# Optimization experiments

Measured on AMD Instinct MI355X. Metric: run time of the kernel, lower is better.

## Reference

```python
import jax, jax.numpy as jnp
import numpy as np

USER_NUM = 200000
ITEM_NUM = 100000
EMB = 64
N_LAYERS = 2
NE_S = 3200000
NE_R = 3200000


def setup_inputs() -> dict:
    key = jax.random.key(0)
    ks = jax.random.split(key, 10)
    scale = 1.0 / np.sqrt(EMB)
    user_emb = jax.random.normal(ks[0], (USER_NUM, EMB), jnp.float32) * scale
    item_emb = jax.random.normal(ks[1], (ITEM_NUM, EMB), jnp.float32) * scale
    # torch Linear weight is [out_features, in_features] = [EMB, 2*EMB]
    W = jax.random.normal(ks[2], (N_LAYERS, EMB, 2 * EMB), jnp.float32) * (1.0 / np.sqrt(2 * EMB))
    b = jnp.zeros((N_LAYERS, EMB), jnp.float32)
    s_rows = jax.random.randint(ks[3], (NE_S,), 0, USER_NUM, jnp.int32)
    s_cols = jax.random.randint(ks[4], (NE_S,), 0, USER_NUM, jnp.int32)
    s_vals = jax.random.uniform(ks[5], (NE_S,), jnp.float32) / 16.0  # ~row-normalized
    r_rows = jax.random.randint(ks[6], (NE_R,), 0, USER_NUM, jnp.int32)
    r_cols = jax.random.randint(ks[7], (NE_R,), 0, ITEM_NUM, jnp.int32)
    r_vals = jax.random.uniform(ks[8], (NE_R,), jnp.float32) / 16.0
    return {"user_emb": user_emb, "item_emb": item_emb, "W": W, "b": b,
            "s_rows": s_rows, "s_cols": s_cols, "s_vals": s_vals,
            "r_rows": r_rows, "r_cols": r_cols, "r_vals": r_vals}


def _spmm(rows, cols, vals, X, n_rows):
    # COO sparse [n_rows, n_cols] @ dense X[n_cols, d]
    return jax.ops.segment_sum(vals[:, None] * X[cols], rows, num_segments=n_rows)


def reference(user_emb, item_emb, W, b, s_rows, s_cols, s_vals, r_rows, r_cols, r_vals):
    U = user_emb
    V = item_emb
    for i in range(N_LAYERS):
        agg = _spmm(s_rows, s_cols, s_vals, U, USER_NUM)      # [U, EMB]
        h = jnp.concatenate([agg, U], axis=1)                 # [U, 2*EMB]
        U = jax.nn.relu(h @ W[i].T + b[i])                    # [U, EMB]
    user_all = U + _spmm(r_rows, r_cols, r_vals, V, USER_NUM)
    item_all = V
    return (user_all, item_all)
```

## Files before the change

kernel.cpp:

```cpp
#include <hip/hip_runtime.h>

#define USER_NUM 200000
#define ITEM_NUM 100000
#define EMB 64

#define SCAN_T 256
#define SCAN_E 8
#define SCAN_TILE (SCAN_T * SCAN_E)

__global__ __launch_bounds__(256) void hist_kernel(
    const int* __restrict__ rows, int nnz, int* __restrict__ cnt)
{
    int e = blockIdx.x * 256 + threadIdx.x;
    if (e >= nnz) return;
    atomicAdd(&cnt[rows[e]], 1);
}

__global__ __launch_bounds__(SCAN_T) void block_sum_kernel(
    const int* __restrict__ cnt, int n, int* __restrict__ partials)
{
    __shared__ int sm[SCAN_T];
    int tid = threadIdx.x;
    int base = blockIdx.x * SCAN_TILE + tid * SCAN_E;
    int s = 0;
    #pragma unroll
    for (int j = 0; j < SCAN_E; ++j) {
        int i = base + j;
        if (i < n) s += cnt[i];
    }
    sm[tid] = s; __syncthreads();
    for (int off = SCAN_T / 2; off > 0; off >>= 1) {
        if (tid < off) sm[tid] += sm[tid + off];
        __syncthreads();
    }
    if (tid == 0) partials[blockIdx.x] = sm[0];
}

__global__ __launch_bounds__(SCAN_T) void scan_partials_kernel(
    int* __restrict__ partials, int nblocks)
{
    __shared__ int sm[SCAN_T];
    int tid = threadIdx.x;
    int v = (tid < nblocks) ? partials[tid] : 0;
    sm[tid] = v; __syncthreads();
    for (int off = 1; off < SCAN_T; off <<= 1) {
        int a = (tid >= off) ? sm[tid - off] : 0;
        __syncthreads();
        sm[tid] += a;
        __syncthreads();
    }
    if (tid < nblocks) partials[tid] = sm[tid] - v;
}

__global__ __launch_bounds__(SCAN_T) void scan_tile_kernel(
    const int* __restrict__ cnt, int n, const int* __restrict__ partials,
    int* __restrict__ row_ptr, int* __restrict__ cursor)
{
    __shared__ int sm[SCAN_T];
    int tid = threadIdx.x;
    int base = blockIdx.x * SCAN_TILE + tid * SCAN_E;
    int local[SCAN_E];
    int s = 0;
    #pragma unroll
    for (int j = 0; j < SCAN_E; ++j) {
        int i = base + j;
        local[j] = (i < n) ? cnt[i] : 0;
        s += local[j];
    }
    sm[tid] = s; __syncthreads();
    for (int off = 1; off < SCAN_T; off <<= 1) {
        int a = (tid >= off) ? sm[tid - off] : 0;
        __syncthreads();
        sm[tid] += a;
        __syncthreads();
    }
    int run = partials[blockIdx.x] + (sm[tid] - s);
    #pragma unroll
    for (int j = 0; j < SCAN_E; ++j) {
        int i = base + j;
        if (i < n) { row_ptr[i] = run; cursor[i] = run; }
        run += local[j];
        if (i == n - 1) row_ptr[n] = run;
    }
}

__global__ __launch_bounds__(256) void scatter_kernel(
    const int* __restrict__ rows, const int* __restrict__ cols,
    const float* __restrict__ vals, int nnz,
    int* __restrict__ cursor, int2* __restrict__ epairs)
{
    int e = blockIdx.x * 256 + threadIdx.x;
    if (e >= nnz) return;
    int r = rows[e];
    int p = atomicAdd(&cursor[r], 1);
    epairs[p] = make_int2(cols[e], __float_as_int(vals[e]));
}

__global__ __launch_bounds__(256) void spmm_csr_kernel(
    const int* __restrict__ row_ptr, const int2* __restrict__ epairs,
    const float* __restrict__ X, const float* __restrict__ addin,
    float* __restrict__ out, int n_rows)
{
    int gid = blockIdx.x * 256 + threadIdx.x;
    int row = gid >> 6;
    int lane = gid & 63;
    if (row >= n_rows) return;
    int beg = row_ptr[row], end = row_ptr[row + 1];
    float acc = addin ? addin[(size_t)row * EMB + lane] : 0.0f;
    int i = beg;
    for (; i + 4 <= end; i += 4) {
        int2 e0 = epairs[i], e1 = epairs[i+1], e2 = epairs[i+2], e3 = epairs[i+3];
        float x0 = X[(size_t)e0.x * EMB + lane];
        float x1 = X[(size_t)e1.x * EMB + lane];
        float x2 = X[(size_t)e2.x * EMB + lane];
        float x3 = X[(size_t)e3.x * EMB + lane];
        acc = fmaf(__int_as_float(e0.y), x0, acc);
        acc = fmaf(__int_as_float(e1.y), x1, acc);
        acc = fmaf(__int_as_float(e2.y), x2, acc);
        acc = fmaf(__int_as_float(e3.y), x3, acc);
    }
    for (; i < end; ++i) {
        int2 e = epairs[i];
        acc = fmaf(__int_as_float(e.y), X[(size_t)e.x * EMB + lane], acc);
    }
    out[(size_t)row * EMB + lane] = acc;
}

__global__ __launch_bounds__(256) void spmm_atomic_kernel(
    const int* __restrict__ rows, const int* __restrict__ cols,
    const float* __restrict__ vals, const float* __restrict__ X,
    float* __restrict__ out, int nnz)
{
    int t = blockIdx.x * 256 + threadIdx.x;
    int e = t >> 4;
    if (e >= nnz) return;
    int q = (t & 15) << 2;
    int r = rows[e];
    int c = cols[e];
    float v = vals[e];
    float4 x = *reinterpret_cast<const float4*>(X + (size_t)c * EMB + q);
    float* o = out + (size_t)r * EMB + q;
    atomicAdd(o + 0, v * x.x);
    atomicAdd(o + 1, v * x.y);
    atomicAdd(o + 2, v * x.z);
    atomicAdd(o + 3, v * x.w);
}

#define DENSE_BLOCKS 512
#define DENSE_SPAN (DENSE_BLOCKS * 256)

__global__ __launch_bounds__(256, 2) void dense_relu_kernel(
    const float* __restrict__ agg, const float* __restrict__ Uin,
    const float* __restrict__ W,
    const float* __restrict__ bias,
    float* __restrict__ Uout, int nrows)
{
    __shared__ float Wl[64 * 128 + 64];
    int tid = threadIdx.x;
    #pragma unroll
    for (int i = 0; i < 8; ++i) {
        int idx = tid + i * 256;
        reinterpret_cast<float4*>(Wl)[idx] = reinterpret_cast<const float4*>(W)[idx];
    }
    if (tid < 64) Wl[8192 + tid] = bias[tid];
    __syncthreads();

    int gid = blockIdx.x * 256 + tid;
    int u0 = gid;
    int u1 = gid + DENSE_SPAN;
    bool ok1 = (u1 < nrows);
    if (u0 >= nrows) return;

    float acc[2][EMB];
    #pragma unroll
    for (int k = 0; k < EMB; ++k) {
        float bv = Wl[8192 + k];
        acc[0][k] = bv;
        acc[1][k] = bv;
    }

    #pragma unroll 1
    for (int half = 0; half < 2; ++half) {
        const float* __restrict__ src = half ? Uin : agg;
        const float4* r0 = reinterpret_cast<const float4*>(src + (size_t)u0 * EMB);
        const float4* r1 = ok1 ? reinterpret_cast<const float4*>(src + (size_t)u1 * EMB)
                               : r0;
        #pragma unroll 1
        for (int jq = 0; jq < 16; ++jq) {
            float4 h0 = r0[jq];
            float4 h1 = r1[jq];
            #pragma unroll
            for (int k = 0; k < EMB; ++k) {
                float4 wv = *reinterpret_cast<const float4*>(
                    Wl + k * 128 + half * 64 + jq * 4);
                acc[0][k] = fmaf(h0.x, wv.x, acc[0][k]);
                acc[0][k] = fmaf(h0.y, wv.y, acc[0][k]);
                acc[0][k] = fmaf(h0.z, wv.z, acc[0][k]);
                acc[0][k] = fmaf(h0.w, wv.w, acc[0][k]);
                acc[1][k] = fmaf(h1.x, wv.x, acc[1][k]);
                acc[1][k] = fmaf(h1.y, wv.y, acc[1][k]);
                acc[1][k] = fmaf(h1.z, wv.z, acc[1][k]);
                acc[1][k] = fmaf(h1.w, wv.w, acc[1][k]);
            }
        }
    }

    {
        float* orow = Uout + (size_t)u0 * EMB;
        #pragma unroll
        for (int q = 0; q < 16; ++q) {
            float4 o;
            o.x = fmaxf(acc[0][q*4+0], 0.f);
            o.y = fmaxf(acc[0][q*4+1], 0.f);
            o.z = fmaxf(acc[0][q*4+2], 0.f);
            o.w = fmaxf(acc[0][q*4+3], 0.f);
            reinterpret_cast<float4*>(orow)[q] = o;
        }
    }
    if (ok1) {
        float* orow = Uout + (size_t)u1 * EMB;
        #pragma unroll
        for (int q = 0; q < 16; ++q) {
            float4 o;
            o.x = fmaxf(acc[1][q*4+0], 0.f);
            o.y = fmaxf(acc[1][q*4+1], 0.f);
            o.z = fmaxf(acc[1][q*4+2], 0.f);
            o.w = fmaxf(acc[1][q*4+3], 0.f);
            reinterpret_cast<float4*>(orow)[q] = o;
        }
    }
}

static void build_csr(const int* rows, const int* cols, const float* vals,
                      int nnz, int n_rows, int* cnt, int* partials,
                      int* row_ptr, int2* epairs, hipStream_t stream)
{
    int nScan = (n_rows + SCAN_TILE - 1) / SCAN_TILE;
    hipMemsetAsync(cnt, 0, (size_t)n_rows * sizeof(int), stream);
    hist_kernel<<<(nnz + 255) / 256, 256, 0, stream>>>(rows, nnz, cnt);
    block_sum_kernel<<<nScan, SCAN_T, 0, stream>>>(cnt, n_rows, partials);
    scan_partials_kernel<<<1, SCAN_T, 0, stream>>>(partials, nScan);
    scan_tile_kernel<<<nScan, SCAN_T, 0, stream>>>(cnt, n_rows, partials,
                                                   row_ptr, cnt);
    scatter_kernel<<<(nnz + 255) / 256, 256, 0, stream>>>(rows, cols, vals, nnz,
                                                          cnt, epairs);
}

extern "C" void kernel_launch(void* const* d_in, const int* in_sizes, int n_in,
                              void* d_out, int out_size, void* d_ws, size_t ws_size,
                              hipStream_t stream) {
    const float* user_emb = (const float*)d_in[0];
    const float* item_emb = (const float*)d_in[1];
    const float* W        = (const float*)d_in[2];
    const float* b        = (const float*)d_in[3];
    const int*   s_rows   = (const int*)d_in[4];
    const int*   s_cols   = (const int*)d_in[5];
    const float* s_vals   = (const float*)d_in[6];
    const int*   r_rows   = (const int*)d_in[7];
    const int*   r_cols   = (const int*)d_in[8];
    const float* r_vals   = (const float*)d_in[9];

    int ne_s = in_sizes[4];
    int ne_r = in_sizes[7];

    float* out      = (float*)d_out;
    float* user_out = out;
    float* item_out = out + (size_t)USER_NUM * EMB;

    char* w = (char*)d_ws;
    float* agg      = (float*)w;  w += (size_t)USER_NUM * EMB * 4;
    int*   s_rowptr = (int*)w;    w += (size_t)(USER_NUM + 1) * 4;
    int*   r_rowptr = (int*)w;    w += (size_t)(USER_NUM + 1) * 4;
    int*   cnt      = (int*)w;    w += (size_t)USER_NUM * 4;
    int*   partials = (int*)w;    w += 256 * 4;
    int2*  s_epairs = (int2*)w;   w += (size_t)ne_s * 8;
    int2*  r_epairs = (int2*)w;   w += (size_t)ne_r * 8;
    size_t needed = (size_t)(w - (char*)d_ws);

    size_t aggBytes = (size_t)USER_NUM * EMB * sizeof(float);
    int spmmBlocks  = (USER_NUM * 64 + 255) / 256;

    if (ws_size >= needed) {
        build_csr(s_rows, s_cols, s_vals, ne_s, USER_NUM,
                  cnt, partials, s_rowptr, s_epairs, stream);
        build_csr(r_rows, r_cols, r_vals, ne_r, USER_NUM,
                  cnt, partials, r_rowptr, r_epairs, stream);

        spmm_csr_kernel<<<spmmBlocks, 256, 0, stream>>>(
            s_rowptr, s_epairs, user_emb, nullptr, agg, USER_NUM);
        dense_relu_kernel<<<DENSE_BLOCKS, 256, 0, stream>>>(
            agg, user_emb, W, b, user_out, USER_NUM);

        spmm_csr_kernel<<<spmmBlocks, 256, 0, stream>>>(
            s_rowptr, s_epairs, user_out, nullptr, agg, USER_NUM);
        dense_relu_kernel<<<DENSE_BLOCKS, 256, 0, stream>>>(
            agg, user_out, W + 64 * 128, b + 64, user_out, USER_NUM);

        spmm_csr_kernel<<<spmmBlocks, 256, 0, stream>>>(
            r_rowptr, r_epairs, item_emb, user_out, user_out, USER_NUM);
    } else {
        int spmmBlocksS = (ne_s * 16 + 255) / 256;
        int spmmBlocksR = (ne_r * 16 + 255) / 256;
        hipMemsetAsync(agg, 0, aggBytes, stream);
        spmm_atomic_kernel<<<spmmBlocksS, 256, 0, stream>>>(s_rows, s_cols, s_vals,
                                                            user_emb, agg, ne_s);
        dense_relu_kernel<<<DENSE_BLOCKS, 256, 0, stream>>>(agg, user_emb, W, b,
                                                            user_out, USER_NUM);
        hipMemsetAsync(agg, 0, aggBytes, stream);
        spmm_atomic_kernel<<<spmmBlocksS, 256, 0, stream>>>(s_rows, s_cols, s_vals,
                                                            user_out, agg, ne_s);
        dense_relu_kernel<<<DENSE_BLOCKS, 256, 0, stream>>>(agg, user_out,
                                                            W + 64 * 128, b + 64,
                                                            user_out, USER_NUM);
        spmm_atomic_kernel<<<spmmBlocksR, 256, 0, stream>>>(r_rows, r_cols, r_vals,
                                                            item_emb, user_out, ne_r);
    }

    hipMemcpyAsync(item_out, item_emb, (size_t)ITEM_NUM * EMB * sizeof(float),
                   hipMemcpyDeviceToDevice, stream);
}
```

Measured before the change: 1.538 ms.

## Replace per-row CSR build with 256-row bucket partition and LDS-accumulating SpMM

Replaces the full per-row CSR construction (global histogram, multi-kernel scan, global-atomic scatter) with a coarse bucketing of edges into 256-row groups. A block-local partition kernel stages edges in LDS and writes them out contiguously per bucket, packing the local row index into the column word. SpMM then gives one block per bucket and accumulates into a 64 KB shared-memory tile with LDS atomics. This cuts global atomics and scattered writes during preprocessing, but adds shared-atomic contention and lower occupancy in the SpMM.

```diff
diff --git a/kernel.cpp b/kernel.cpp
--- a/kernel.cpp
+++ b/kernel.cpp
@@ -4,126 +4,160 @@
 #define ITEM_NUM 100000
 #define EMB 64
 
-#define SCAN_T 256
-#define SCAN_E 8
-#define SCAN_TILE (SCAN_T * SCAN_E)
-
-__global__ __launch_bounds__(256) void hist_kernel(
-    const int* __restrict__ rows, int nnz, int* __restrict__ cnt)
-{
-    int e = blockIdx.x * 256 + threadIdx.x;
-    if (e >= nnz) return;
-    atomicAdd(&cnt[rows[e]], 1);
-}
-
-__global__ __launch_bounds__(SCAN_T) void block_sum_kernel(
-    const int* __restrict__ cnt, int n, int* __restrict__ partials)
-{
-    __shared__ int sm[SCAN_T];
+#define BROWS 256
+#define NB ((USER_NUM + BROWS - 1) / BROWS)
+#define PTILE 8192
+#define PTHREADS 512
+#define COLMASK 0x3FFFFu
+
+__global__ __launch_bounds__(256) void bucket_hist_kernel(
+    const int* __restrict__ rows, int nnz, int* __restrict__ gcnt)
+{
+    __shared__ int h[NB];
+    for (int i = threadIdx.x; i < NB; i += 256) h[i] = 0;
+    __syncthreads();
+    int stride = gridDim.x * 256;
+    for (int e = blockIdx.x * 256 + threadIdx.x; e < nnz; e += stride)
+        atomicAdd(&h[rows[e] >> 8], 1);
+    __syncthreads();
+    for (int i = threadIdx.x; i < NB; i += 256) {
+        int v = h[i];
+        if (v) atomicAdd(&gcnt[i], v);
+    }
+}
+
+__global__ __launch_bounds__(1024) void scan_buckets_kernel(
+    const int* __restrict__ gcnt, int* __restrict__ gbase,
+    int* __restrict__ gcursor)
+{
+    __shared__ int sm[1024];
     int tid = threadIdx.x;
-    int base = blockIdx.x * SCAN_TILE + tid * SCAN_E;
-    int s = 0;
-    #pragma unroll
-    for (int j = 0; j < SCAN_E; ++j) {
-        int i = base + j;
-        if (i < n) s += cnt[i];
-    }
-    sm[tid] = s; __syncthreads();
-    for (int off = SCAN_T / 2; off > 0; off >>= 1) {
-        if (tid < off) sm[tid] += sm[tid + off];
-        __syncthreads();
-    }
-    if (tid == 0) partials[blockIdx.x] = sm[0];
-}
-
-__global__ __launch_bounds__(SCAN_T) void scan_partials_kernel(
-    int* __restrict__ partials, int nblocks)
-{
-    __shared__ int sm[SCAN_T];
-    int tid = threadIdx.x;
-    int v = (tid < nblocks) ? partials[tid] : 0;
+    int v = (tid < NB) ? gcnt[tid] : 0;
     sm[tid] = v; __syncthreads();
-    for (int off = 1; off < SCAN_T; off <<= 1) {
+    for (int off = 1; off < 1024; off <<= 1) {
         int a = (tid >= off) ? sm[tid - off] : 0;
         __syncthreads();
         sm[tid] += a;
         __syncthreads();
     }
-    if (tid < nblocks) partials[tid] = sm[tid] - v;
-}
-
-__global__ __launch_bounds__(SCAN_T) void scan_tile_kernel(
-    const int* __restrict__ cnt, int n, const int* __restrict__ partials,
-    int* __restrict__ row_ptr, int* __restrict__ cursor)
-{
-    __shared__ int sm[SCAN_T];
-    int tid = threadIdx.x;
-    int base = blockIdx.x * SCAN_TILE + tid * SCAN_E;
-    int local[SCAN_E];
-    int s = 0;
-    #pragma unroll
-    for (int j = 0; j < SCAN_E; ++j) {
-        int i = base + j;
-        local[j] = (i < n) ? cnt[i] : 0;
-        s += local[j];
-    }
-    sm[tid] = s; __syncthreads();
-    for (int off = 1; off < SCAN_T; off <<= 1) {
-        int a = (tid >= off) ? sm[tid - off] : 0;
-        __syncthreads();
-        sm[tid] += a;
-        __syncthreads();
-    }
-    int run = partials[blockIdx.x] + (sm[tid] - s);
-    #pragma unroll
-    for (int j = 0; j < SCAN_E; ++j) {
-        int i = base + j;
-        if (i < n) { row_ptr[i] = run; cursor[i] = run; }
-        run += local[j];
-        if (i == n - 1) row_ptr[n] = run;
-    }
-}
-
-__global__ __launch_bounds__(256) void scatter_kernel(
+    if (tid < NB) {
+        int excl = sm[tid] - v;
+        gbase[tid] = excl;
+        gcursor[tid] = excl;
+        if (tid == NB - 1) gbase[NB] = sm[tid];
+    }
+}
+
+__global__ __launch_bounds__(PTHREADS) void partition_kernel(
     const int* __restrict__ rows, const int* __restrict__ cols,
     const float* __restrict__ vals, int nnz,
-    int* __restrict__ cursor, int2* __restrict__ epairs)
-{
-    int e = blockIdx.x * 256 + threadIdx.x;
-    if (e >= nnz) return;
-    int r = rows[e];
-    int p = atomicAdd(&cursor[r], 1);
-    epairs[p] = make_int2(cols[e], __float_as_int(vals[e]));
-}
-
-__global__ __launch_bounds__(256) void spmm_csr_kernel(
-    const int* __restrict__ row_ptr, const int2* __restrict__ epairs,
+    int* __restrict__ gcursor, uint2* __restrict__ epart)
+{
+    __shared__ int hist[NB];
+    __shared__ int cur[NB];
+    __shared__ int gbaseb[NB];
+    __shared__ int psum[PTHREADS];
+    extern __shared__ char dyn[];
+    uint2* stage = (uint2*)dyn;
+    unsigned short* sb = (unsigned short*)(dyn + PTILE * 8);
+
+    int tid = threadIdx.x;
+    int base = blockIdx.x * PTILE;
+    int cnt = nnz - base; if (cnt > PTILE) cnt = PTILE;
+
+    for (int i = tid; i < NB; i += PTHREADS) { hist[i] = 0; cur[i] = 0; }
+    __syncthreads();
+
+    for (int k = tid; k < cnt; k += PTHREADS)
+        atomicAdd(&hist[rows[base + k] >> 8], 1);
+    __syncthreads();
+
+    int b0 = tid * 2, b1 = tid * 2 + 1;
+    int h0 = (b0 < NB) ? hist[b0] : 0;
+    int h1 = (b1 < NB) ? hist[b1] : 0;
+    int s = h0 + h1;
+    psum[tid] = s; __syncthreads();
+    for (int off = 1; off < PTHREADS; off <<= 1) {
+        int a = (tid >= off) ? psum[tid - off] : 0;
+        __syncthreads();
+        psum[tid] += a;
+        __syncthreads();
+    }
+    int run = psum[tid] - s;
+    if (b0 < NB) hist[b0] = run;
+    if (b1 < NB) hist[b1] = run + h0;
+    if (b0 < NB && h0 > 0) gbaseb[b0] = atomicAdd(&gcursor[b0], h0);
+    if (b1 < NB && h1 > 0) gbaseb[b1] = atomicAdd(&gcursor[b1], h1);
+    __syncthreads();
+
+    for (int k = tid; k < cnt; k += PTHREADS) {
+        int e = base + k;
+        int r = rows[e];
+        int b = r >> 8;
+        unsigned int packed = ((unsigned)(r & 255) << 18) | (unsigned)cols[e];
+        int pos = hist[b] + atomicAdd(&cur[b], 1);
+        stage[pos] = make_uint2(packed, __float_as_uint(vals[e]));
+        sb[pos] = (unsigned short)b;
+    }
+    __syncthreads();
+
+    for (int j = tid; j < cnt; j += PTHREADS) {
+        int b = sb[j];
+        epart[gbaseb[b] + (j - hist[b])] = stage[j];
+    }
+}
+
+__global__ __launch_bounds__(256, 2) void spmm_bucket_kernel(
+    const int* __restrict__ gbase, const uint2* __restrict__ epart,
     const float* __restrict__ X, const float* __restrict__ addin,
     float* __restrict__ out, int n_rows)
 {
-    int gid = blockIdx.x * 256 + threadIdx.x;
-    int row = gid >> 6;
-    int lane = gid & 63;
-    if (row >= n_rows) return;
-    int beg = row_ptr[row], end = row_ptr[row + 1];
-    float acc = addin ? addin[(size_t)row * EMB + lane] : 0.0f;
-    int i = beg;
-    for (; i + 4 <= end; i += 4) {
-        int2 e0 = epairs[i], e1 = epairs[i+1], e2 = epairs[i+2], e3 = epairs[i+3];
-        float x0 = X[(size_t)e0.x * EMB + lane];
-        float x1 = X[(size_t)e1.x * EMB + lane];
-        float x2 = X[(size_t)e2.x * EMB + lane];
-        float x3 = X[(size_t)e3.x * EMB + lane];
-        acc = fmaf(__int_as_float(e0.y), x0, acc);
-        acc = fmaf(__int_as_float(e1.y), x1, acc);
-        acc = fmaf(__int_as_float(e2.y), x2, acc);
-        acc = fmaf(__int_as_float(e3.y), x3, acc);
-    }
-    for (; i < end; ++i) {
-        int2 e = epairs[i];
-        acc = fmaf(__int_as_float(e.y), X[(size_t)e.x * EMB + lane], acc);
-    }
-    out[(size_t)row * EMB + lane] = acc;
+    __shared__ float acc[BROWS * EMB];
+    int tid = threadIdx.x;
+    int b = blockIdx.x;
+    int row0 = b << 8;
+
+    #pragma unroll
+    for (int i = 0; i < 16; ++i)
+        reinterpret_cast<float4*>(acc)[tid + i * 256] = make_float4(0, 0, 0, 0);
+    __syncthreads();
+
+    int beg = gbase[b], end = gbase[b + 1];
+    int wid = tid >> 6, lane = tid & 63;
+
+    int i = beg + wid;
+    for (; i + 12 < end; i += 16) {
+        uint2 e0 = epart[i];
+        uint2 e1 = epart[i + 4];
+        uint2 e2 = epart[i + 8];
+        uint2 e3 = epart[i + 12];
+        float x0 = X[(size_t)(e0.x & COLMASK) * EMB + lane];
+        float x1 = X[(size_t)(e1.x & COLMASK) * EMB + lane];
+        float x2 = X[(size_t)(e2.x & COLMASK) * EMB + lane];
+        float x3 = X[(size_t)(e3.x & COLMASK) * EMB + lane];
+        atomicAdd(&acc[(e0.x >> 18) * EMB + lane], __uint_as_float(e0.y) * x0);
+        atomicAdd(&acc[(e1.x >> 18) * EMB + lane], __uint_as_float(e1.y) * x1);
+        atomicAdd(&acc[(e2.x >> 18) * EMB + lane], __uint_as_float(e2.y) * x2);
+        atomicAdd(&acc[(e3.x >> 18) * EMB + lane], __uint_as_float(e3.y) * x3);
+    }
+    for (; i < end; i += 4) {
+        uint2 e0 = epart[i];
+        float x0 = X[(size_t)(e0.x & COLMASK) * EMB + lane];
+        atomicAdd(&acc[(e0.x >> 18) * EMB + lane], __uint_as_float(e0.y) * x0);
+    }
+    __syncthreads();
+
+    int nr = n_rows - row0; if (nr > BROWS) nr = BROWS;
+    int totalf4 = nr * (EMB / 4);
+    for (int f = tid; f < totalf4; f += 256) {
+        float4 v = reinterpret_cast<const float4*>(acc)[f];
+        size_t g = (size_t)row0 * (EMB / 4) + f;
+        if (addin) {
+            float4 a = reinterpret_cast<const float4*>(addin)[g];
+            v.x += a.x; v.y += a.y; v.z += a.z; v.w += a.w;
+        }
+        reinterpret_cast<float4*>(out)[g] = v;
+    }
 }
 
 __global__ __launch_bounds__(256) void spmm_atomic_kernel(
@@ -231,19 +265,16 @@
     }
 }
 
-static void build_csr(const int* rows, const int* cols, const float* vals,
-                      int nnz, int n_rows, int* cnt, int* partials,
-                      int* row_ptr, int2* epairs, hipStream_t stream)
-{
-    int nScan = (n_rows + SCAN_TILE - 1) / SCAN_TILE;
-    hipMemsetAsync(cnt, 0, (size_t)n_rows * sizeof(int), stream);
-    hist_kernel<<<(nnz + 255) / 256, 256, 0, stream>>>(rows, nnz, cnt);
-    block_sum_kernel<<<nScan, SCAN_T, 0, stream>>>(cnt, n_rows, partials);
-    scan_partials_kernel<<<1, SCAN_T, 0, stream>>>(partials, nScan);
-    scan_tile_kernel<<<nScan, SCAN_T, 0, stream>>>(cnt, n_rows, partials,
-                                                   row_ptr, cnt);
-    scatter_kernel<<<(nnz + 255) / 256, 256, 0, stream>>>(rows, cols, vals, nnz,
-                                                          cnt, epairs);
+static void build_buckets(const int* rows, const int* cols, const float* vals,
+                          int nnz, int* gcnt, int* gbase, int* gcursor,
+                          uint2* epart, hipStream_t stream)
+{
+    hipMemsetAsync(gcnt, 0, NB * sizeof(int), stream);
+    bucket_hist_kernel<<<1024, 256, 0, stream>>>(rows, nnz, gcnt);
+    scan_buckets_kernel<<<1, 1024, 0, stream>>>(gcnt, gbase, gcursor);
+    int ptiles = (nnz + PTILE - 1) / PTILE;
+    partition_kernel<<<ptiles, PTHREADS, PTILE * 10, stream>>>(
+        rows, cols, vals, nnz, gcursor, epart);
 }
 
 extern "C" void kernel_launch(void* const* d_in, const int* in_sizes, int n_in,
@@ -269,35 +300,34 @@
 
     char* w = (char*)d_ws;
     float* agg      = (float*)w;  w += (size_t)USER_NUM * EMB * 4;
-    int*   s_rowptr = (int*)w;    w += (size_t)(USER_NUM + 1) * 4;
-    int*   r_rowptr = (int*)w;    w += (size_t)(USER_NUM + 1) * 4;
-    int*   cnt      = (int*)w;    w += (size_t)USER_NUM * 4;
-    int*   partials = (int*)w;    w += 256 * 4;
-    int2*  s_epairs = (int2*)w;   w += (size_t)ne_s * 8;
-    int2*  r_epairs = (int2*)w;   w += (size_t)ne_r * 8;
+    uint2* s_part   = (uint2*)w;  w += (size_t)ne_s * 8;
+    uint2* r_part   = (uint2*)w;  w += (size_t)ne_r * 8;
+    int*   gcnt     = (int*)w;    w += (size_t)NB * 4;
+    int*   gbase_s  = (int*)w;    w += (size_t)(NB + 1) * 4;
+    int*   gbase_r  = (int*)w;    w += (size_t)(NB + 1) * 4;
+    int*   gcursor  = (int*)w;    w += (size_t)NB * 4;
     size_t needed = (size_t)(w - (char*)d_ws);
 
     size_t aggBytes = (size_t)USER_NUM * EMB * sizeof(float);
-    int spmmBlocks  = (USER_NUM * 64 + 255) / 256;
 
     if (ws_size >= needed) {
-        build_csr(s_rows, s_cols, s_vals, ne_s, USER_NUM,
-                  cnt, partials, s_rowptr, s_epairs, stream);
-        build_csr(r_rows, r_cols, r_vals, ne_r, USER_NUM,
-                  cnt, partials, r_rowptr, r_epairs, stream);
-
-        spmm_csr_kernel<<<spmmBlocks, 256, 0, stream>>>(
-            s_rowptr, s_epairs, user_emb, nullptr, agg, USER_NUM);
+        build_buckets(s_rows, s_cols, s_vals, ne_s, gcnt, gbase_s, gcursor,
+                      s_part, stream);
+        build_buckets(r_rows, r_cols, r_vals, ne_r, gcnt, gbase_r, gcursor,
+                      r_part, stream);
+
+        spmm_bucket_kernel<<<NB, 256, 0, stream>>>(
+            gbase_s, s_part, user_emb, nullptr, agg, USER_NUM);
         dense_relu_kernel<<<DENSE_BLOCKS, 256, 0, stream>>>(
             agg, user_emb, W, b, user_out, USER_NUM);
 
-        spmm_csr_kernel<<<spmmBlocks, 256, 0, stream>>>(
-            s_rowptr, s_epairs, user_out, nullptr, agg, USER_NUM);
+        spmm_bucket_kernel<<<NB, 256, 0, stream>>>(
+            gbase_s, s_part, user_out, nullptr, agg, USER_NUM);
         dense_relu_kernel<<<DENSE_BLOCKS, 256, 0, stream>>>(
             agg, user_out, W + 64 * 128, b + 64, user_out, USER_NUM);
 
-        spmm_csr_kernel<<<spmmBlocks, 256, 0, stream>>>(
-            r_rowptr, r_epairs, item_emb, user_out, user_out, USER_NUM);
+        spmm_bucket_kernel<<<NB, 256, 0, stream>>>(
+            gbase_r, r_part, item_emb, user_out, user_out, USER_NUM);
     } else {
         int spmmBlocksS = (ne_s * 16 + 255) / 256;
         int spmmBlocksR = (ne_r * 16 + 255) / 256;
```

After: 4.527 ms. +194.4%, slower.
